# Optimization experiments

Hardware: AMD Instinct MI355X
Metric: run time of the kernel (lower is better)

Reference implementation:

```python
import jax, jax.numpy as jnp
import numpy as np

N_NODES = 50000
N_EDGES = 800000
D = 64


def _gcn_conv(x, row, col, edge_weight, W, b):
    # degree via scatter-add of edge weights onto source nodes (row)
    deg = jax.ops.segment_sum(edge_weight, row, num_segments=x.shape[0])
    deg_inv_sqrt = jnp.where(deg > 0, jax.lax.rsqrt(deg), 0.0)  # inf -> 0
    norm = deg_inv_sqrt[row] * edge_weight * deg_inv_sqrt[col]  # [E]
    h = x @ W + b                                               # [N, out]
    msg = norm[:, None] * h[row]                                # gather + scale, [E, out]
    # PyG 'add' aggregation onto target nodes (col)
    return jax.ops.segment_sum(msg, col, num_segments=x.shape[0])


def setup_inputs() -> dict:
    key = jax.random.key(0)
    ks = jax.random.split(key, 5)
    x = jax.random.normal(ks[0], (N_NODES, D), dtype=jnp.float32)
    edge_index = jax.random.randint(ks[1], (2, N_EDGES), 0, N_NODES, dtype=jnp.int64)
    edge_weight = jax.random.uniform(ks[2], (N_EDGES,), dtype=jnp.float32)
    s = 1.0 / np.sqrt(D)
    W1 = jax.random.normal(ks[3], (D, D), dtype=jnp.float32) * s
    b1 = jnp.zeros((D,), dtype=jnp.float32)
    W2 = jax.random.normal(ks[4], (D, D), dtype=jnp.float32) * s
    b2 = jnp.zeros((D,), dtype=jnp.float32)
    return {"x": x, "edge_index": edge_index, "edge_weight": edge_weight,
            "W1": W1, "b1": b1, "W2": W2, "b2": b2}


def reference(x, edge_index, edge_weight, W1, b1, W2, b2):
    row, col = edge_index[0], edge_index[1]
    h = _gcn_conv(x, row, col, edge_weight, W1, b1)
    h = jax.nn.relu(h)  # dropout is identity in eval mode
    h = _gcn_conv(h, row, col, edge_weight, W2, b2)
    return h
```

## Files before the change

### kernel.cpp

```cpp
#include <hip/hip_runtime.h>
#include <hip/hip_fp16.h>

#define NNODES 50000
#define NEDGES 800000
#define DIM 64
#define CAP 64

#define NBUCK 196
#define EPB 3200
#define NCH 250
#define MAXB 6144
#define CASTB (NNODES * 16 / 256)
#define GROUPS (NNODES / 8)

__global__ __launch_bounds__(256) void p1_kernel(const int* __restrict__ ei,
                                                 unsigned int* __restrict__ ch,
                                                 unsigned int* __restrict__ rh,
                                                 const float* __restrict__ x,
                                                 __half* __restrict__ xs) {
    int bid = blockIdx.x;
    int tid = threadIdx.x;
    if (bid >= NCH) {
        int i = (bid - NCH) * 256 + tid;
        float4 v = ((const float4*)x)[i];
        __half2 p0 = __float22half2_rn(make_float2(v.x, v.y));
        __half2 p1 = __float22half2_rn(make_float2(v.z, v.w));
        uint2 u;
        u.x = *(unsigned int*)&p0;
        u.y = *(unsigned int*)&p1;
        ((uint2*)xs)[i] = u;
        return;
    }
    __shared__ unsigned int hc[NBUCK], hr[NBUCK];
    if (tid < NBUCK) { hc[tid] = 0u; hr[tid] = 0u; }
    __syncthreads();
    int base = bid * EPB;
    for (int i = tid; i < EPB; i += 256) {
        int r = ei[base + i];
        int c = ei[NEDGES + base + i];
        atomicAdd(&hc[c >> 8], 1u);
        atomicAdd(&hr[r >> 8], 1u);
    }
    __syncthreads();
    if (tid < NBUCK) {
        ch[tid * NCH + bid] = hc[tid];
        rh[tid * NCH + bid] = hr[tid];
    }
}

__global__ __launch_bounds__(256) void p2_scan(unsigned int* __restrict__ ch,
                                               unsigned int* __restrict__ rh,
                                               unsigned int* __restrict__ tot) {
    int j = blockIdx.x;
    unsigned int* h = (j < NBUCK) ? (ch + j * NCH) : (rh + (j - NBUCK) * NCH);
    int tid = threadIdx.x;
    int lane = tid & 63, wv = tid >> 6;
    unsigned int v = (tid < NCH) ? h[tid] : 0u;
    unsigned int s = v;
#pragma unroll
    for (int d = 1; d < 64; d <<= 1) {
        unsigned int t = __shfl_up(s, d);
        if (lane >= d) s += t;
    }
    __shared__ unsigned int wsum[4];
    if (lane == 63) wsum[wv] = s;
    __syncthreads();
    unsigned int off = 0;
    for (int k = 0; k < wv; k++) off += wsum[k];
    if (tid < NCH) h[tid] = off + s - v;
    if (tid == 255) tot[j] = off + s;
}

__global__ __launch_bounds__(256) void p3_scatter(const int* __restrict__ ei,
                                                  const float* __restrict__ ew,
                                                  const unsigned int* __restrict__ ch,
                                                  const unsigned int* __restrict__ rh,
                                                  unsigned long long* __restrict__ recc,
                                                  unsigned long long* __restrict__ recr) {
    __shared__ unsigned int rc[NBUCK], rr[NBUCK];
    int tid = threadIdx.x, bid = blockIdx.x;
    if (tid < NBUCK) {
        rc[tid] = ch[tid * NCH + bid];
        rr[tid] = rh[tid * NCH + bid];
    }
    __syncthreads();
    int base = bid * EPB;
    for (int i = tid; i < EPB; i += 256) {
        int r = ei[base + i];
        int c = ei[NEDGES + base + i];
        float w = ew[base + i];
        unsigned int hw = (unsigned int)__half_as_ushort(__float2half(w));
        unsigned int pc = atomicAdd(&rc[c >> 8], 1u);
        recc[(size_t)(c >> 8) * MAXB + pc] =
            (unsigned long long)(unsigned int)r |
            ((unsigned long long)(c & 255) << 16) |
            ((unsigned long long)hw << 32);
        unsigned int pr = atomicAdd(&rr[r >> 8], 1u);
        recr[(size_t)(r >> 8) * MAXB + pr] =
            (unsigned long long)(r & 255) |
            ((unsigned long long)__float_as_uint(w) << 32);
    }
}

__global__ __launch_bounds__(256) void p4_build(const unsigned long long* __restrict__ recc,
                                                const unsigned long long* __restrict__ recr,
                                                const unsigned int* __restrict__ tot,
                                                unsigned int* __restrict__ edata,
                                                int* __restrict__ cnt,
                                                float* __restrict__ deg) {
    int bid = blockIdx.x, tid = threadIdx.x;
    if (bid < NBUCK) {
        __shared__ unsigned int c256[256];
        c256[tid] = 0u;
        __syncthreads();
        int n = (int)tot[bid];
        const unsigned long long* rb = recc + (size_t)bid * MAXB;
        for (int i = tid; i < n; i += 256) {
            unsigned long long rec = rb[i];
            unsigned int r = (unsigned int)rec & 0xFFFFu;
            unsigned int cl = ((unsigned int)rec >> 16) & 0xFFu;
            unsigned int hw = (unsigned int)(rec >> 32) & 0xFFFFu;
            unsigned int pos = atomicAdd(&c256[cl], 1u);
            if (pos < CAP) edata[(unsigned)((bid << 8) + cl) * CAP + pos] = r | (hw << 16);
        }
        __syncthreads();
        int node = (bid << 8) + tid;
        if (node < NNODES) cnt[node] = (int)c256[tid];
    } else {
        int b = bid - NBUCK;
        __shared__ float d256[256];
        d256[tid] = 0.f;
        __syncthreads();
        int n = (int)tot[NBUCK + b];
        const unsigned long long* rb = recr + (size_t)b * MAXB;
        for (int i = tid; i < n; i += 256) {
            unsigned long long rec = rb[i];
            unsigned int rl = (unsigned int)rec & 0xFFu;
            float w = __uint_as_float((unsigned int)(rec >> 32));
            atomicAdd(&d256[rl], w);
        }
        __syncthreads();
        int node = (b << 8) + tid;
        if (node < NNODES) deg[node] = d256[tid];
    }
}

__device__ __forceinline__ void store_out(__half* O, int i, float v) {
    O[i] = __float2half(v);
}
__device__ __forceinline__ void store_out(float* O, int i, float v) { O[i] = v; }

__device__ __forceinline__ float rsq0(float d) {
    return (d > 0.f) ? rsqrtf(d) : 0.f;
}

template <bool IS_L1, typename OutT>
__global__ __launch_bounds__(256) void layer_kernel(const int* __restrict__ cnt,
                                                    const unsigned int* __restrict__ edata,
                                                    const __half* __restrict__ HS,
                                                    const float* __restrict__ deg,
                                                    float* __restrict__ qbuf,
                                                    const float* __restrict__ W,
                                                    const float* __restrict__ b,
                                                    OutT* __restrict__ O) {
    __shared__ float Wsh[64 * 64];
    __shared__ float Ls[8][64];

    const int tid = threadIdx.x;
    {
        const float4* Wv = (const float4*)W;
        float4* Wd = (float4*)Wsh;
#pragma unroll
        for (int i = 0; i < 4; i++) Wd[tid + 256 * i] = Wv[tid + 256 * i];
    }

    const int wave = tid >> 6;
    const int lane = tid & 63;
    const int h = lane >> 5;
    const int hl = lane & 31;
    const int sub = hl >> 3;
    const int sl = hl & 7;
    const int hbit = lane & 32;
    const uint4* __restrict__ H16 = (const uint4*)HS;
    const float blane = b[lane];

    const int na = blockIdx.x * 8 + wave * 2;
    const int node = na + h;

    int m = cnt[node];
    if (m > CAP) m = CAP;
    unsigned int dw = 0, dw2 = 0;
    if (hl < m) dw = edata[node * CAP + hl];
    if (32 + hl < m) dw2 = edata[node * CAP + 32 + hl];

    float acc[8];
#pragma unroll
    for (int k = 0; k < 8; k++) acc[k] = 0.f;
    float p = 0.f;

    auto group4 = [&](unsigned int dwx, int tb) {
        unsigned int u0 = (unsigned int)__shfl((int)dwx, hbit | (4 * (tb + 0) + sub));
        unsigned int u1 = (unsigned int)__shfl((int)dwx, hbit | (4 * (tb + 1) + sub));
        unsigned int u2 = (unsigned int)__shfl((int)dwx, hbit | (4 * (tb + 2) + sub));
        unsigned int u3 = (unsigned int)__shfl((int)dwx, hbit | (4 * (tb + 3) + sub));
        int r0 = u0 & 0xFFFFu, r1 = u1 & 0xFFFFu, r2 = u2 & 0xFFFFu, r3 = u3 & 0xFFFFu;
        uint4 h0 = H16[r0 * 8 + sl];
        uint4 h1 = H16[r1 * 8 + sl];
        uint4 h2 = H16[r2 * 8 + sl];
        uint4 h3 = H16[r3 * 8 + sl];
        float nd0 = __half2float(__ushort_as_half((unsigned short)(u0 >> 16)));
        float nd1 = __half2float(__ushort_as_half((unsigned short)(u1 >> 16)));
        float nd2 = __half2float(__ushort_as_half((unsigned short)(u2 >> 16)));
        float nd3 = __half2float(__ushort_as_half((unsigned short)(u3 >> 16)));
        if (IS_L1) {
            nd0 *= rsq0(deg[r0]);
            nd1 *= rsq0(deg[r1]);
            nd2 *= rsq0(deg[r2]);
            nd3 *= rsq0(deg[r3]);
            p += nd0 + nd1 + nd2 + nd3;
        }
        const __half2* c0 = (const __half2*)&h0;
        const __half2* c1 = (const __half2*)&h1;
        const __half2* c2 = (const __half2*)&h2;
        const __half2* c3 = (const __half2*)&h3;
#pragma unroll
        for (int k = 0; k < 4; k++) {
            float2 f0 = __half22float2(c0[k]);
            float2 f1 = __half22float2(c1[k]);
            float2 f2 = __half22float2(c2[k]);
            float2 f3 = __half22float2(c3[k]);
            acc[2 * k + 0] = fmaf(nd0, f0.x, acc[2 * k + 0]);
            acc[2 * k + 1] = fmaf(nd0, f0.y, acc[2 * k + 1]);
            acc[2 * k + 0] = fmaf(nd1, f1.x, acc[2 * k + 0]);
            acc[2 * k + 1] = fmaf(nd1, f1.y, acc[2 * k + 1]);
            acc[2 * k + 0] = fmaf(nd2, f2.x, acc[2 * k + 0]);
            acc[2 * k + 1] = fmaf(nd2, f2.y, acc[2 * k + 1]);
            acc[2 * k + 0] = fmaf(nd3, f3.x, acc[2 * k + 0]);
            acc[2 * k + 1] = fmaf(nd3, f3.y, acc[2 * k + 1]);
        }
    };

    if (m <= 16) {
        group4(dw, 0);
    } else if (m <= 32) {
        group4(dw, 0);
        group4(dw, 4);
    } else {
        group4(dw, 0);
        group4(dw, 4);
        group4(dw2, 0);
        group4(dw2, 4);
    }

#pragma unroll
    for (int mask = 8; mask <= 16; mask <<= 1) {
#pragma unroll
        for (int k = 0; k < 8; k++) acc[k] += __shfl_xor(acc[k], mask);
        if (IS_L1) p += __shfl_xor(p, mask);
    }

    if (sub == 0) {
        *(float4*)&Ls[wave * 2 + h][8 * sl + 0] = make_float4(acc[0], acc[1], acc[2], acc[3]);
        *(float4*)&Ls[wave * 2 + h][8 * sl + 4] = make_float4(acc[4], acc[5], acc[6], acc[7]);
    }

    float qa, qb;
    if (IS_L1) {
        qa = __shfl(p, 0);
        qb = __shfl(p, 32);
        if (lane == 0) qbuf[na] = qa;
        if (lane == 32) qbuf[na + 1] = qb;
    } else {
        qa = qbuf[na];
        qb = qbuf[na + 1];
    }
    __syncthreads();

    float oa = qa * blane;
    float ob = qb * blane;
#pragma unroll
    for (int f4 = 0; f4 < 16; f4++) {
        float4 Aa = *(const float4*)&Ls[wave * 2 + 0][4 * f4];
        float4 Ab = *(const float4*)&Ls[wave * 2 + 1][4 * f4];
        float w0 = Wsh[(4 * f4 + 0) * 64 + lane];
        float w1 = Wsh[(4 * f4 + 1) * 64 + lane];
        float w2 = Wsh[(4 * f4 + 2) * 64 + lane];
        float w3 = Wsh[(4 * f4 + 3) * 64 + lane];
        oa = fmaf(Aa.x, w0, oa); ob = fmaf(Ab.x, w0, ob);
        oa = fmaf(Aa.y, w1, oa); ob = fmaf(Ab.y, w1, ob);
        oa = fmaf(Aa.z, w2, oa); ob = fmaf(Ab.z, w2, ob);
        oa = fmaf(Aa.w, w3, oa); ob = fmaf(Ab.w, w3, ob);
    }

    float da = rsq0(deg[na]);
    float db = rsq0(deg[na + 1]);
    float za = da * oa, zb = db * ob;
    if (IS_L1) {
        za = fmaxf(za, 0.f);
        zb = fmaxf(zb, 0.f);
        store_out(O, na * DIM + lane, da * za);
        store_out(O, (na + 1) * DIM + lane, db * zb);
    } else {
        store_out(O, na * DIM + lane, za);
        store_out(O, (na + 1) * DIM + lane, zb);
    }
}

extern "C" void kernel_launch(void* const* d_in, const int* in_sizes, int n_in,
                              void* d_out, int out_size, void* d_ws, size_t ws_size,
                              hipStream_t stream) {
    const float* x  = (const float*)d_in[0];
    const int*   ei = (const int*)d_in[1];
    const float* ew = (const float*)d_in[2];
    const float* W1 = (const float*)d_in[3];
    const float* b1 = (const float*)d_in[4];
    const float* W2 = (const float*)d_in[5];
    const float* b2 = (const float*)d_in[6];
    float* out = (float*)d_out;

    const int N = NNODES;

    char* ws = (char*)d_ws;
    size_t off = 0;
    auto alloc = [&](size_t bytes) { char* p = ws + off; off += (bytes + 255) & ~size_t(255); return p; };
    float*        deg   = (float*)alloc((size_t)N * 4);
    int*          cnt   = (int*)  alloc((size_t)N * 4);
    unsigned int* edata = (unsigned int*)alloc((size_t)N * CAP * 4);
    float*        qbuf  = (float*)alloc((size_t)N * 4);
    __half*       xs    = (__half*)alloc((size_t)N * DIM * 2);
    __half*       h1s   = (__half*)alloc((size_t)N * DIM * 2);
    unsigned int* ch    = (unsigned int*)alloc((size_t)NBUCK * NCH * 4);
    unsigned int* rh    = (unsigned int*)alloc((size_t)NBUCK * NCH * 4);
    unsigned int* tot   = (unsigned int*)alloc((size_t)2 * NBUCK * 4);
    unsigned long long* recr = (unsigned long long*)alloc((size_t)NBUCK * MAXB * 8);
    unsigned long long* recc = (unsigned long long*)d_out;

    p1_kernel<<<NCH + CASTB, 256, 0, stream>>>(ei, ch, rh, x, xs);
    p2_scan<<<2 * NBUCK, 256, 0, stream>>>(ch, rh, tot);
    p3_scatter<<<NCH, 256, 0, stream>>>(ei, ew, ch, rh, recc, recr);
    p4_build<<<2 * NBUCK, 256, 0, stream>>>(recc, recr, tot, edata, cnt, deg);

    layer_kernel<true, __half><<<GROUPS, 256, 0, stream>>>(cnt, edata, xs, deg, qbuf, W1, b1, h1s);
    layer_kernel<false, float><<<GROUPS, 256, 0, stream>>>(cnt, edata, h1s, deg, qbuf, W2, b2, out);
}
```

Before: 163.2 us.

## Prescale features by source norm and precompute bias coefficients in build phase

Splits the build kernel into a row-degree pass that writes inverse square-root degrees and a column pass that also accumulates the per-node bias coefficient q. The x-to-half cast moves into the column pass and premultiplies each row by its dis value, so layer 1 no longer gathers deg[r] per edge. The layer kernel also gets a two-edge group to trim padded work for nodes with 17-24 edges. This adds one more launch and serializes the cast behind the degree computation, and the column pass now does a random dis[r] read per edge.

```diff
diff --git a/kernel.cpp b/kernel.cpp
--- a/kernel.cpp
+++ b/kernel.cpp
@@ -13,25 +13,11 @@
 #define CASTB (NNODES * 16 / 256)
 #define GROUPS (NNODES / 8)
 
-__global__ __launch_bounds__(256) void p1_kernel(const int* __restrict__ ei,
-                                                 unsigned int* __restrict__ ch,
-                                                 unsigned int* __restrict__ rh,
-                                                 const float* __restrict__ x,
-                                                 __half* __restrict__ xs) {
-    int bid = blockIdx.x;
-    int tid = threadIdx.x;
-    if (bid >= NCH) {
-        int i = (bid - NCH) * 256 + tid;
-        float4 v = ((const float4*)x)[i];
-        __half2 p0 = __float22half2_rn(make_float2(v.x, v.y));
-        __half2 p1 = __float22half2_rn(make_float2(v.z, v.w));
-        uint2 u;
-        u.x = *(unsigned int*)&p0;
-        u.y = *(unsigned int*)&p1;
-        ((uint2*)xs)[i] = u;
-        return;
-    }
+__global__ __launch_bounds__(256) void p1_hist(const int* __restrict__ ei,
+                                               unsigned int* __restrict__ ch,
+                                               unsigned int* __restrict__ rh) {
     __shared__ unsigned int hc[NBUCK], hr[NBUCK];
+    int tid = threadIdx.x, bid = blockIdx.x;
     if (tid < NBUCK) { hc[tid] = 0u; hr[tid] = 0u; }
     __syncthreads();
     int base = bid * EPB;
@@ -102,46 +88,72 @@
     }
 }
 
-__global__ __launch_bounds__(256) void p4_build(const unsigned long long* __restrict__ recc,
-                                                const unsigned long long* __restrict__ recr,
-                                                const unsigned int* __restrict__ tot,
-                                                unsigned int* __restrict__ edata,
-                                                int* __restrict__ cnt,
-                                                float* __restrict__ deg) {
+__device__ __forceinline__ float rsq0(float d) {
+    return (d > 0.f) ? rsqrtf(d) : 0.f;
+}
+
+__global__ __launch_bounds__(256) void p4_row(const unsigned long long* __restrict__ recr,
+                                              const unsigned int* __restrict__ tot,
+                                              float* __restrict__ dis) {
+    __shared__ float d256[256];
+    int tid = threadIdx.x, bid = blockIdx.x;
+    d256[tid] = 0.f;
+    __syncthreads();
+    int n = (int)tot[NBUCK + bid];
+    const unsigned long long* rb = recr + (size_t)bid * MAXB;
+    for (int i = tid; i < n; i += 256) {
+        unsigned long long rec = rb[i];
+        atomicAdd(&d256[(unsigned int)rec & 0xFFu],
+                  __uint_as_float((unsigned int)(rec >> 32)));
+    }
+    __syncthreads();
+    int node = (bid << 8) + tid;
+    if (node < NNODES) dis[node] = rsq0(d256[tid]);
+}
+
+__global__ __launch_bounds__(256) void p4_col(const unsigned long long* __restrict__ recc,
+                                              const unsigned int* __restrict__ tot,
+                                              const float* __restrict__ dis,
+                                              unsigned int* __restrict__ edata,
+                                              int* __restrict__ cnt,
+                                              float* __restrict__ qbuf,
+                                              const float* __restrict__ x,
+                                              __half* __restrict__ xs) {
     int bid = blockIdx.x, tid = threadIdx.x;
-    if (bid < NBUCK) {
-        __shared__ unsigned int c256[256];
-        c256[tid] = 0u;
-        __syncthreads();
-        int n = (int)tot[bid];
-        const unsigned long long* rb = recc + (size_t)bid * MAXB;
-        for (int i = tid; i < n; i += 256) {
-            unsigned long long rec = rb[i];
-            unsigned int r = (unsigned int)rec & 0xFFFFu;
-            unsigned int cl = ((unsigned int)rec >> 16) & 0xFFu;
-            unsigned int hw = (unsigned int)(rec >> 32) & 0xFFFFu;
-            unsigned int pos = atomicAdd(&c256[cl], 1u);
-            if (pos < CAP) edata[(unsigned)((bid << 8) + cl) * CAP + pos] = r | (hw << 16);
-        }
-        __syncthreads();
-        int node = (bid << 8) + tid;
-        if (node < NNODES) cnt[node] = (int)c256[tid];
-    } else {
-        int b = bid - NBUCK;
-        __shared__ float d256[256];
-        d256[tid] = 0.f;
-        __syncthreads();
-        int n = (int)tot[NBUCK + b];
-        const unsigned long long* rb = recr + (size_t)b * MAXB;
-        for (int i = tid; i < n; i += 256) {
-            unsigned long long rec = rb[i];
-            unsigned int rl = (unsigned int)rec & 0xFFu;
-            float w = __uint_as_float((unsigned int)(rec >> 32));
-            atomicAdd(&d256[rl], w);
-        }
-        __syncthreads();
-        int node = (b << 8) + tid;
-        if (node < NNODES) deg[node] = d256[tid];
+    if (bid >= NBUCK) {
+        int i = (bid - NBUCK) * 256 + tid;
+        float d = dis[i >> 4];
+        float4 v = ((const float4*)x)[i];
+        __half2 p0 = __float22half2_rn(make_float2(v.x * d, v.y * d));
+        __half2 p1 = __float22half2_rn(make_float2(v.z * d, v.w * d));
+        uint2 u;
+        u.x = *(unsigned int*)&p0;
+        u.y = *(unsigned int*)&p1;
+        ((uint2*)xs)[i] = u;
+        return;
+    }
+    __shared__ unsigned int c256[256];
+    __shared__ float q256[256];
+    c256[tid] = 0u;
+    q256[tid] = 0.f;
+    __syncthreads();
+    int n = (int)tot[bid];
+    const unsigned long long* rb = recc + (size_t)bid * MAXB;
+    for (int i = tid; i < n; i += 256) {
+        unsigned long long rec = rb[i];
+        unsigned int r = (unsigned int)rec & 0xFFFFu;
+        unsigned int cl = ((unsigned int)rec >> 16) & 0xFFu;
+        unsigned int hw = (unsigned int)(rec >> 32) & 0xFFFFu;
+        unsigned int pos = atomicAdd(&c256[cl], 1u);
+        if (pos < CAP) edata[(unsigned)((bid << 8) + cl) * CAP + pos] = r | (hw << 16);
+        atomicAdd(&q256[cl],
+                  __half2float(__ushort_as_half((unsigned short)hw)) * dis[r]);
+    }
+    __syncthreads();
+    int node = (bid << 8) + tid;
+    if (node < NNODES) {
+        cnt[node] = (int)c256[tid];
+        qbuf[node] = q256[tid];
     }
 }
 
@@ -149,17 +161,13 @@
     O[i] = __float2half(v);
 }
 __device__ __forceinline__ void store_out(float* O, int i, float v) { O[i] = v; }
-
-__device__ __forceinline__ float rsq0(float d) {
-    return (d > 0.f) ? rsqrtf(d) : 0.f;
-}
 
 template <bool IS_L1, typename OutT>
 __global__ __launch_bounds__(256) void layer_kernel(const int* __restrict__ cnt,
                                                     const unsigned int* __restrict__ edata,
                                                     const __half* __restrict__ HS,
-                                                    const float* __restrict__ deg,
-                                                    float* __restrict__ qbuf,
+                                                    const float* __restrict__ dis,
+                                                    const float* __restrict__ qbuf,
                                                     const float* __restrict__ W,
                                                     const float* __restrict__ b,
                                                     OutT* __restrict__ O) {
@@ -196,7 +204,6 @@
     float acc[8];
 #pragma unroll
     for (int k = 0; k < 8; k++) acc[k] = 0.f;
-    float p = 0.f;
 
     auto group4 = [&](unsigned int dwx, int tb) {
         unsigned int u0 = (unsigned int)__shfl((int)dwx, hbit | (4 * (tb + 0) + sub));
@@ -212,13 +219,6 @@
         float nd1 = __half2float(__ushort_as_half((unsigned short)(u1 >> 16)));
         float nd2 = __half2float(__ushort_as_half((unsigned short)(u2 >> 16)));
         float nd3 = __half2float(__ushort_as_half((unsigned short)(u3 >> 16)));
-        if (IS_L1) {
-            nd0 *= rsq0(deg[r0]);
-            nd1 *= rsq0(deg[r1]);
-            nd2 *= rsq0(deg[r2]);
-            nd3 *= rsq0(deg[r3]);
-            p += nd0 + nd1 + nd2 + nd3;
-        }
         const __half2* c0 = (const __half2*)&h0;
         const __half2* c1 = (const __half2*)&h1;
         const __half2* c2 = (const __half2*)&h2;
@@ -240,23 +240,41 @@
         }
     };
 
-    if (m <= 16) {
-        group4(dw, 0);
-    } else if (m <= 32) {
-        group4(dw, 0);
-        group4(dw, 4);
-    } else {
-        group4(dw, 0);
-        group4(dw, 4);
+    auto group2 = [&](unsigned int dwx, int tb) {
+        unsigned int u0 = (unsigned int)__shfl((int)dwx, hbit | (4 * (tb + 0) + sub));
+        unsigned int u1 = (unsigned int)__shfl((int)dwx, hbit | (4 * (tb + 1) + sub));
+        int r0 = u0 & 0xFFFFu, r1 = u1 & 0xFFFFu;
+        uint4 h0 = H16[r0 * 8 + sl];
+        uint4 h1 = H16[r1 * 8 + sl];
+        float nd0 = __half2float(__ushort_as_half((unsigned short)(u0 >> 16)));
+        float nd1 = __half2float(__ushort_as_half((unsigned short)(u1 >> 16)));
+        const __half2* c0 = (const __half2*)&h0;
+        const __half2* c1 = (const __half2*)&h1;
+#pragma unroll
+        for (int k = 0; k < 4; k++) {
+            float2 f0 = __half22float2(c0[k]);
+            float2 f1 = __half22float2(c1[k]);
+            acc[2 * k + 0] = fmaf(nd0, f0.x, acc[2 * k + 0]);
+            acc[2 * k + 1] = fmaf(nd0, f0.y, acc[2 * k + 1]);
+            acc[2 * k + 0] = fmaf(nd1, f1.x, acc[2 * k + 0]);
+            acc[2 * k + 1] = fmaf(nd1, f1.y, acc[2 * k + 1]);
+        }
+    };
+
+    group4(dw, 0);
+    if (m > 16) {
+        if (m <= 24) group2(dw, 4);
+        else group4(dw, 4);
+    }
+    if (m > 32) {
         group4(dw2, 0);
-        group4(dw2, 4);
+        if (m > 48) group4(dw2, 4);
     }
 
 #pragma unroll
     for (int mask = 8; mask <= 16; mask <<= 1) {
 #pragma unroll
         for (int k = 0; k < 8; k++) acc[k] += __shfl_xor(acc[k], mask);
-        if (IS_L1) p += __shfl_xor(p, mask);
     }
 
     if (sub == 0) {
@@ -264,16 +282,8 @@
         *(float4*)&Ls[wave * 2 + h][8 * sl + 4] = make_float4(acc[4], acc[5], acc[6], acc[7]);
     }
 
-    float qa, qb;
-    if (IS_L1) {
-        qa = __shfl(p, 0);
-        qb = __shfl(p, 32);
-        if (lane == 0) qbuf[na] = qa;
-        if (lane == 32) qbuf[na + 1] = qb;
-    } else {
-        qa = qbuf[na];
-        qb = qbuf[na + 1];
-    }
+    const float qa = qbuf[na];
+    const float qb = qbuf[na + 1];
     __syncthreads();
 
     float oa = qa * blane;
@@ -292,8 +302,8 @@
         oa = fmaf(Aa.w, w3, oa); ob = fmaf(Ab.w, w3, ob);
     }
 
-    float da = rsq0(deg[na]);
-    float db = rsq0(deg[na + 1]);
+    float da = dis[na];
+    float db = dis[na + 1];
     float za = da * oa, zb = db * ob;
     if (IS_L1) {
         za = fmaxf(za, 0.f);
@@ -323,7 +333,7 @@
     char* ws = (char*)d_ws;
     size_t off = 0;
     auto alloc = [&](size_t bytes) { char* p = ws + off; off += (bytes + 255) & ~size_t(255); return p; };
-    float*        deg   = (float*)alloc((size_t)N * 4);
+    float*        dis   = (float*)alloc((size_t)N * 4);
     int*          cnt   = (int*)  alloc((size_t)N * 4);
     unsigned int* edata = (unsigned int*)alloc((size_t)N * CAP * 4);
     float*        qbuf  = (float*)alloc((size_t)N * 4);
@@ -335,11 +345,12 @@
     unsigned long long* recr = (unsigned long long*)alloc((size_t)NBUCK * MAXB * 8);
     unsigned long long* recc = (unsigned long long*)d_out;
 
-    p1_kernel<<<NCH + CASTB, 256, 0, stream>>>(ei, ch, rh, x, xs);
+    p1_hist<<<NCH, 256, 0, stream>>>(ei, ch, rh);
     p2_scan<<<2 * NBUCK, 256, 0, stream>>>(ch, rh, tot);
     p3_scatter<<<NCH, 256, 0, stream>>>(ei, ew, ch, rh, recc, recr);
-    p4_build<<<2 * NBUCK, 256, 0, stream>>>(recc, recr, tot, edata, cnt, deg);
-
-    layer_kernel<true, __half><<<GROUPS, 256, 0, stream>>>(cnt, edata, xs, deg, qbuf, W1, b1, h1s);
-    layer_kernel<false, float><<<GROUPS, 256, 0, stream>>>(cnt, edata, h1s, deg, qbuf, W2, b2, out);
-}
+    p4_row<<<NBUCK, 256, 0, stream>>>(recr, tot, dis);
+    p4_col<<<NBUCK + CASTB, 256, 0, stream>>>(recc, tot, dis, edata, cnt, qbuf, x, xs);
+
+    layer_kernel<true, __half><<<GROUPS, 256, 0, stream>>>(cnt, edata, xs, dis, qbuf, W1, b1, h1s);
+    layer_kernel<false, float><<<GROUPS, 256, 0, stream>>>(cnt, edata, h1s, dis, qbuf, W2, b2, out);
+}
```

After: 165.9 us. Within noise of the previous version (+1.6%).
